# Kernel tuning notes

Hardware: AMD Instinct MI355X
Metric: run time of the kernel (lower is better)

The kernel has to match this reference:

```python
import jax, jax.numpy as jnp
import numpy as np

B = 65536
D_IN = 512
H = 512
EPS = 1e-5


def _layernorm(x, gamma, beta):
    # matches torch ref: unbiased std (ddof=1), eps added to std (not var)
    mean = jnp.mean(x, axis=-1, keepdims=True)
    std = jnp.std(x, axis=-1, ddof=1, keepdims=True)
    return gamma * (x - mean) / (std + EPS) + beta


def setup_inputs() -> dict:
    key = jax.random.key(0)
    ks = jax.random.split(key, 16)
    fan_in = D_IN + H
    s = 1.0 / np.sqrt(fan_in)
    inp = {
        "x": jax.random.normal(ks[0], (B, D_IN), dtype=jnp.float32),
        "prev_h": jax.random.normal(ks[1], (B, H), dtype=jnp.float32),
        "prev_c": jax.random.normal(ks[2], (B, H), dtype=jnp.float32),
        # torch Linear: weight [out, in], bias [out]
        "Wf": jax.random.uniform(ks[3], (H, fan_in), jnp.float32, -s, s),
        "bf": jax.random.uniform(ks[4], (H,), jnp.float32, -s, s),
        "Wi": jax.random.uniform(ks[5], (H, fan_in), jnp.float32, -s, s),
        "bi": jax.random.uniform(ks[6], (H,), jnp.float32, -s, s),
        "Wo": jax.random.uniform(ks[7], (H, fan_in), jnp.float32, -s, s),
        "bo": jax.random.uniform(ks[8], (H,), jnp.float32, -s, s),
        "Wj": jax.random.uniform(ks[9], (H, fan_in), jnp.float32, -s, s),
        "bj": jax.random.uniform(ks[10], (H,), jnp.float32, -s, s),
        "gamma_f": jnp.ones((H,), jnp.float32),
        "beta_f": jnp.zeros((H,), jnp.float32),
        "gamma_i": jnp.ones((H,), jnp.float32),
        "beta_i": jnp.zeros((H,), jnp.float32),
        "gamma_o": jnp.ones((H,), jnp.float32),
        "beta_o": jnp.zeros((H,), jnp.float32),
        "gamma_j": jnp.ones((H,), jnp.float32),
        "beta_j": jnp.zeros((H,), jnp.float32),
        "gamma_c": jnp.ones((H,), jnp.float32),
        "beta_c": jnp.zeros((H,), jnp.float32),
    }
    return inp


def reference(x, prev_h, prev_c, Wf, bf, Wi, bi, Wo, bo, Wj, bj,
              gamma_f, beta_f, gamma_i, beta_i, gamma_o, beta_o,
              gamma_j, beta_j, gamma_c, beta_c):
    combined = jnp.concatenate([x, prev_h], axis=-1)  # [B, D_IN+H]
    ft = jax.nn.sigmoid(_layernorm(combined @ Wf.T + bf, gamma_f, beta_f))
    it = jax.nn.sigmoid(_layernorm(combined @ Wi.T + bi, gamma_i, beta_i))
    ot = jax.nn.sigmoid(_layernorm(combined @ Wo.T + bo, gamma_o, beta_o))
    jt = jnp.tanh(_layernorm(combined @ Wj.T + bj, gamma_j, beta_j))
    c = ft * prev_c + jnp.minimum(1.0 - ft, it) * jt
    c = _layernorm(c, gamma_c, beta_c)
    h = ot * c
    return (h, c)
```

## Files before the change

### kernel.cpp

```cpp
#include <hip/hip_runtime.h>
#include <math.h>

#define B_ROWS 65536
#define D_IN   512
#define HDIM   512
#define FAN    1024
#define NCOL   2048
#define EPS    1e-5f

#define BM 256
#define BN 256
#define BK 64
#define KTILES (FAN / BK)
#define NITER  (KTILES / 2)
#define TILES_PER_BLK 4

typedef unsigned short u16;
using bfrag = __attribute__((ext_vector_type(8))) short;
using facc  = __attribute__((ext_vector_type(4))) float;
using us4   = __attribute__((ext_vector_type(4))) unsigned short;
using us8   = __attribute__((ext_vector_type(8))) unsigned short;

static __device__ __forceinline__ u16 f2b(float f) {
    unsigned u = __builtin_bit_cast(unsigned, f);
    u += 0x7fffu + ((u >> 16) & 1u);
    return (u16)(u >> 16);
}
static __device__ __forceinline__ float b2f(u16 h) {
    unsigned u = ((unsigned)h) << 16;
    return __builtin_bit_cast(float, u);
}
static __device__ __forceinline__ void gload16(const u16* g, u16* l) {
    __builtin_amdgcn_global_load_lds(
        (const __attribute__((address_space(1))) void*)g,
        (__attribute__((address_space(3))) void*)l, 16, 0, 0);
}
static __device__ __forceinline__ void wave_meanrstd(float s, float ss, float& mean, float& rstd)
{
#pragma unroll
    for (int o = 1; o < 64; o <<= 1) { s += __shfl_xor(s, o); ss += __shfl_xor(ss, o); }
    mean = s * (1.f / 512.f);
    float var = (ss - 512.f * mean * mean) * (1.f / 511.f);
    rstd = 1.f / (sqrtf(fmaxf(var, 0.f)) + EPS);
}
static __device__ __forceinline__ float fast_sigmoid(float z) {
    return __fdividef(1.f, 1.f + __expf(-z));
}
static __device__ __forceinline__ float fast_tanh(float z) {
    return __fdividef(2.f, 1.f + __expf(-2.f * z)) - 1.f;
}

__global__ void pack_combined(const float* __restrict__ x, const float* __restrict__ ph,
                              u16* __restrict__ comb)
{
    long i = (long)blockIdx.x * 256 + threadIdx.x;
    if (i >= (long)B_ROWS * D_IN / 4) return;
    long e = i * 4;
    long b = e >> 9;
    int  d = (int)(e & 511);
    float4 xv = *(const float4*)(x + e);
    float4 hv = *(const float4*)(ph + e);
    us4 xb = { f2b(xv.x), f2b(xv.y), f2b(xv.z), f2b(xv.w) };
    us4 hb = { f2b(hv.x), f2b(hv.y), f2b(hv.z), f2b(hv.w) };
    *(us4*)(comb + b * FAN + d)        = xb;
    *(us4*)(comb + b * FAN + D_IN + d) = hb;
}

__global__ void pack_w(const float* __restrict__ Wf, const float* __restrict__ Wi,
                       const float* __restrict__ Wo, const float* __restrict__ Wj,
                       u16* __restrict__ Wall)
{
    long i = (long)blockIdx.x * 256 + threadIdx.x;
    if (i >= (long)NCOL * FAN / 4) return;
    long e = i * 4;
    int  g = (int)(e >> 19);
    long rem = e & 524287L;
    const float* src = (g == 0) ? Wf : (g == 1) ? Wi : (g == 2) ? Wo : Wj;
    float4 v = *(const float4*)(src + rem);
    us4 p = { f2b(v.x), f2b(v.y), f2b(v.z), f2b(v.w) };
    *(us4*)(Wall + e) = p;
}

__global__ void pack_bias(const float* __restrict__ bf_, const float* __restrict__ bi_,
                          const float* __restrict__ bo_, const float* __restrict__ bj_,
                          float* __restrict__ biasAll)
{
    int idx = blockIdx.x * 256 + threadIdx.x;
    if (idx >= NCOL) return;
    int g = idx >> 9;
    const float* s = (g == 0) ? bf_ : (g == 1) ? bi_ : (g == 2) ? bo_ : bj_;
    biasAll[idx] = s[idx & 511];
}

__global__ __launch_bounds__(512)
void gemm_gates(const u16* __restrict__ A, const u16* __restrict__ W,
                const float* __restrict__ biasAll, u16* __restrict__ Cg)
{
    __shared__ u16 lds[2][4][8192];

    const int tid  = threadIdx.x;
    const int lane = tid & 63;
    const int wid  = tid >> 6;
    const int wm   = wid >> 2;
    const int wn   = wid & 3;

    const int nwg = gridDim.x;
    const int swz = (blockIdx.x & 7) * (nwg >> 3) + (blockIdx.x >> 3);
    const long bm  = swz >> 1;
    const int  bn4 = (swz & 1) * TILES_PER_BLK;
    const long arow0 = bm * BM;

    const int sr = tid >> 3;
    const int ss = tid & 7;

    facc acc[8][4];
#pragma unroll
    for (int i = 0; i < 8; ++i)
#pragma unroll
        for (int j = 0; j < 4; ++j) acc[i][j] = facc{0.f, 0.f, 0.f, 0.f};

    auto stageHalf = [&](int buf, int half, int ktg) {
        if (ktg >= TILES_PER_BLK * KTILES) ktg = 0;
        const long k0    = (long)(ktg & (KTILES - 1)) * BK;
        const long bcol0 = ((long)bn4 + (ktg >> 4)) * BN;
#pragma unroll
        for (int i = 0; i < 2; ++i) {
            const int r  = sr + i * 64;
            const int sx = ss ^ (r & 7);
            const u16* src = (half < 2)
                ? (A + (arow0 + half * 128 + r) * (long)FAN + k0 + sx * 8)
                : (W + (bcol0 + (half - 2) * 128 + r) * (long)FAN + k0 + sx * 8);
            gload16(src, &lds[buf][half][i * 4096 + wid * 512]);
        }
    };

    stageHalf(0, 0, 0); stageHalf(0, 1, 0); stageHalf(0, 2, 0); stageHalf(0, 3, 0);
    stageHalf(1, 2, 1); stageHalf(1, 3, 1);
    asm volatile("s_waitcnt vmcnt(4)" ::: "memory");
    __builtin_amdgcn_s_barrier();

    const u16* Ah[2] = { &lds[0][wm][0],            &lds[1][wm][0] };
    const u16* Bh[2] = { &lds[0][2 + (wn >> 1)][0], &lds[1][2 + (wn >> 1)][0] };
    const int lrB0 = (wn & 1) * 64;

#pragma unroll 1
    for (int tile = 0; tile < TILES_PER_BLK; ++tile) {
        const int kb = tile * KTILES;
#pragma unroll 1
        for (int t = 0; t < NITER; ++t) {
            bfrag bq[4][2];
#pragma unroll
            for (int p = 0; p < 8; ++p) {
                const int q  = p & 3;
                const int lt = p >> 2;
                bfrag aq[2][2];
                if (q == 0) {
#pragma unroll
                    for (int nf = 0; nf < 4; ++nf)
#pragma unroll
                        for (int kk = 0; kk < 2; ++kk) {
                            const int lr = lrB0 + nf * 16 + (lane & 15);
                            const int sl = (kk * 4 + (lane >> 4)) ^ (lane & 7);
                            bq[nf][kk] = *(const bfrag*)(Bh[lt] + lr * 64 + sl * 8);
                        }
                }
#pragma unroll
                for (int m2 = 0; m2 < 2; ++m2)
#pragma unroll
                    for (int kk = 0; kk < 2; ++kk) {
                        const int lr = (q * 2 + m2) * 16 + (lane & 15);
                        const int sl = (kk * 4 + (lane >> 4)) ^ (lane & 7);
                        aq[m2][kk] = *(const bfrag*)(Ah[lt] + lr * 64 + sl * 8);
                    }
                if (p == 0)      stageHalf(1, 0, kb + 2 * t + 1);
                else if (p == 1) stageHalf(1, 1, kb + 2 * t + 1);
                else if (p == 2) stageHalf(0, 2, kb + 2 * t + 2);
                else if (p == 3) stageHalf(0, 3, kb + 2 * t + 2);
                else if (p == 4) stageHalf(0, 0, kb + 2 * t + 2);
                else if (p == 5) stageHalf(0, 1, kb + 2 * t + 2);
                else if (p == 6) stageHalf(1, 2, kb + 2 * t + 3);
                else             stageHalf(1, 3, kb + 2 * t + 3);

                if (q == 0) asm volatile("s_waitcnt lgkmcnt(8)" ::: "memory");
                __builtin_amdgcn_s_barrier();
                asm volatile("s_waitcnt lgkmcnt(0)" ::: "memory");
                __builtin_amdgcn_s_setprio(1);
#pragma unroll
                for (int m2 = 0; m2 < 2; ++m2)
#pragma unroll
                    for (int nf = 0; nf < 4; ++nf)
#pragma unroll
                        for (int kk = 0; kk < 2; ++kk)
                            acc[q * 2 + m2][nf] = __builtin_amdgcn_mfma_f32_16x16x32_bf16(
                                bq[nf][kk], aq[m2][kk], acc[q * 2 + m2][nf], 0, 0, 0);
                __builtin_amdgcn_s_setprio(0);
                if (q == 3) asm volatile("s_waitcnt vmcnt(4)" ::: "memory");
                __builtin_amdgcn_s_barrier();
            }
        }

        const long bcol0 = ((long)bn4 + tile) * BN;
#pragma unroll
        for (int nf = 0; nf < 4; ++nf) {
            const long n = bcol0 + wn * 64 + nf * 16 + ((lane >> 4) << 2);
            float4 bv = *(const float4*)(biasAll + n);
#pragma unroll
            for (int mf = 0; mf < 8; ++mf) {
                const long m = arow0 + wm * 128 + mf * 16 + (lane & 15);
                us4 pk = { f2b(acc[mf][nf][0] + bv.x), f2b(acc[mf][nf][1] + bv.y),
                           f2b(acc[mf][nf][2] + bv.z), f2b(acc[mf][nf][3] + bv.w) };
                *(us4*)(Cg + m * (long)NCOL + n) = pk;
                acc[mf][nf] = facc{0.f, 0.f, 0.f, 0.f};
            }
        }
    }
}

__global__ __launch_bounds__(256)
void lstm_act(const u16* __restrict__ pre, const float* __restrict__ pc,
              const float* __restrict__ gf, const float* __restrict__ btf,
              const float* __restrict__ gi, const float* __restrict__ bti,
              const float* __restrict__ go, const float* __restrict__ bto,
              const float* __restrict__ gj, const float* __restrict__ btj,
              const float* __restrict__ gc, const float* __restrict__ btc,
              float* __restrict__ out_h, float* __restrict__ out_c, long rows)
{
    const int  lane = threadIdx.x & 63;
    const int  c0   = lane * 8;
    const long wave = (long)blockIdx.x * 4 + (threadIdx.x >> 6);
    const long totW = (long)gridDim.x * 4;

    const float* gs[4]  = { gf, gi, go, gj };
    const float* bts[4] = { btf, bti, bto, btj };
    float gg[4][8], tt[4][8], gcv[8], tcv[8];
#pragma unroll
    for (int g = 0; g < 4; ++g) {
        *(float4*)&gg[g][0] = *(const float4*)(gs[g] + c0);
        *(float4*)&gg[g][4] = *(const float4*)(gs[g] + c0 + 4);
        *(float4*)&tt[g][0] = *(const float4*)(bts[g] + c0);
        *(float4*)&tt[g][4] = *(const float4*)(bts[g] + c0 + 4);
    }
    *(float4*)&gcv[0] = *(const float4*)(gc + c0);
    *(float4*)&gcv[4] = *(const float4*)(gc + c0 + 4);
    *(float4*)&tcv[0] = *(const float4*)(btc + c0);
    *(float4*)&tcv[4] = *(const float4*)(btc + c0 + 4);

#pragma unroll 1
    for (long row = wave; row < rows; row += totW) {
        float a4[4][8];
#pragma unroll
        for (int g = 0; g < 4; ++g) {
            us8 pv = *(const us8*)(pre + row * NCOL + g * HDIM + c0);
            float y[8];
            float s = 0.f, ssum = 0.f;
#pragma unroll
            for (int e = 0; e < 8; ++e) {
                y[e] = b2f(pv[e]);
                s += y[e]; ssum += y[e] * y[e];
            }
            float mean, rstd;
            wave_meanrstd(s, ssum, mean, rstd);
#pragma unroll
            for (int e = 0; e < 8; ++e) {
                float z = (y[e] - mean) * rstd * gg[g][e] + tt[g][e];
                a4[g][e] = (g == 3) ? fast_tanh(z) : fast_sigmoid(z);
            }
        }

        float4 p0 = *(const float4*)(pc + row * HDIM + c0);
        float4 p1 = *(const float4*)(pc + row * HDIM + c0 + 4);
        float pcv[8] = { p0.x, p0.y, p0.z, p0.w, p1.x, p1.y, p1.z, p1.w };
        float cr[8];
        float s = 0.f, ssum = 0.f;
#pragma unroll
        for (int e = 0; e < 8; ++e) {
            cr[e] = a4[0][e] * pcv[e] + fminf(1.f - a4[0][e], a4[1][e]) * a4[3][e];
            s += cr[e]; ssum += cr[e] * cr[e];
        }
        float mean, rstd;
        wave_meanrstd(s, ssum, mean, rstd);
        float hv[8], cv[8];
#pragma unroll
        for (int e = 0; e < 8; ++e) {
            float cc = (cr[e] - mean) * rstd * gcv[e] + tcv[e];
            cv[e] = cc;
            hv[e] = a4[2][e] * cc;
        }
        *(float4*)(out_h + row * HDIM + c0)     = make_float4(hv[0], hv[1], hv[2], hv[3]);
        *(float4*)(out_h + row * HDIM + c0 + 4) = make_float4(hv[4], hv[5], hv[6], hv[7]);
        *(float4*)(out_c + row * HDIM + c0)     = make_float4(cv[0], cv[1], cv[2], cv[3]);
        *(float4*)(out_c + row * HDIM + c0 + 4) = make_float4(cv[4], cv[5], cv[6], cv[7]);
    }
}

static __device__ __forceinline__ void ln_pair(
    float y0, float y1,
    const float* __restrict__ gam, const float* __restrict__ bet, int c0,
    float* red, int lane, int wid, float& o0, float& o1)
{
    float s = y0 + y1, ss = y0 * y0 + y1 * y1;
#pragma unroll
    for (int o = 32; o; o >>= 1) { s += __shfl_down(s, o); ss += __shfl_down(ss, o); }
    if (lane == 0) { red[wid * 2] = s; red[wid * 2 + 1] = ss; }
    __syncthreads();
    float S  = red[0] + red[2] + red[4] + red[6];
    float SS = red[1] + red[3] + red[5] + red[7];
    __syncthreads();
    float mean = S * (1.f / 512.f);
    float var  = (SS - 512.f * mean * mean) * (1.f / 511.f);
    float rstd = 1.f / (sqrtf(fmaxf(var, 0.f)) + EPS);
    o0 = (y0 - mean) * rstd * gam[c0]     + bet[c0];
    o1 = (y1 - mean) * rstd * gam[c0 + 1] + bet[c0 + 1];
}

__global__ __launch_bounds__(256)
void lstm_naive(const float* __restrict__ x, const float* __restrict__ ph, const float* __restrict__ pc,
                const float* __restrict__ Wf, const float* __restrict__ bf_,
                const float* __restrict__ Wi, const float* __restrict__ bi_,
                const float* __restrict__ Wo, const float* __restrict__ bo_,
                const float* __restrict__ Wj, const float* __restrict__ bj_,
                const float* __restrict__ gf, const float* __restrict__ btf,
                const float* __restrict__ gi, const float* __restrict__ bti,
                const float* __restrict__ go, const float* __restrict__ bto,
                const float* __restrict__ gj, const float* __restrict__ btj,
                const float* __restrict__ gc, const float* __restrict__ btc,
                float* __restrict__ out_h, float* __restrict__ out_c)
{
    __shared__ float comb[FAN];
    __shared__ float red[8];
    const int b = blockIdx.x, t = threadIdx.x;
    const int lane = t & 63, wid = t >> 6;
    for (int k = t; k < D_IN; k += 256) {
        comb[k]        = x[(long)b * D_IN + k];
        comb[D_IN + k] = ph[(long)b * HDIM + k];
    }
    __syncthreads();
    const int c0 = t * 2;
    const float* Ws[4]  = { Wf, Wi, Wo, Wj };
    const float* bs[4]  = { bf_, bi_, bo_, bj_ };
    const float* gs[4]  = { gf, gi, go, gj };
    const float* bts[4] = { btf, bti, bto, btj };
    float a[4][2];
#pragma unroll
    for (int g = 0; g < 4; ++g) {
        float y[2];
#pragma unroll
        for (int e = 0; e < 2; ++e) {
            const float4* w4 = (const float4*)(Ws[g] + (long)(c0 + e) * FAN);
            const float4* c4 = (const float4*)comb;
            float s = 0.f;
            for (int k = 0; k < FAN / 4; ++k) {
                float4 wv = w4[k], cv = c4[k];
                s += wv.x * cv.x + wv.y * cv.y + wv.z * cv.z + wv.w * cv.w;
            }
            y[e] = s + bs[g][c0 + e];
        }
        ln_pair(y[0], y[1], gs[g], bts[g], c0, red, lane, wid, a[g][0], a[g][1]);
        if (g == 3) { a[g][0] = tanhf(a[g][0]); a[g][1] = tanhf(a[g][1]); }
        else        { a[g][0] = 1.f / (1.f + expf(-a[g][0]));
                      a[g][1] = 1.f / (1.f + expf(-a[g][1])); }
    }
    float2 pcv = *(const float2*)(pc + (long)b * HDIM + c0);
    float f0 = a[0][0], i0 = a[1][0], o0 = a[2][0], j0 = a[3][0];
    float f1 = a[0][1], i1 = a[1][1], o1 = a[2][1], j1 = a[3][1];
    float cr0 = f0 * pcv.x + fminf(1.f - f0, i0) * j0;
    float cr1 = f1 * pcv.y + fminf(1.f - f1, i1) * j1;
    float cc0, cc1;
    ln_pair(cr0, cr1, gc, btc, c0, red, lane, wid, cc0, cc1);
    *(float2*)(out_h + (long)b * HDIM + c0) = make_float2(o0 * cc0, o1 * cc1);
    *(float2*)(out_c + (long)b * HDIM + c0) = make_float2(cc0, cc1);
}

extern "C" void kernel_launch(void* const* d_in, const int* in_sizes, int n_in,
                              void* d_out, int out_size, void* d_ws, size_t ws_size,
                              hipStream_t stream)
{
    const float* x   = (const float*)d_in[0];
    const float* ph  = (const float*)d_in[1];
    const float* pc  = (const float*)d_in[2];
    const float* Wf  = (const float*)d_in[3];
    const float* bf_ = (const float*)d_in[4];
    const float* Wi  = (const float*)d_in[5];
    const float* bi_ = (const float*)d_in[6];
    const float* Wo  = (const float*)d_in[7];
    const float* bo_ = (const float*)d_in[8];
    const float* Wj  = (const float*)d_in[9];
    const float* bj_ = (const float*)d_in[10];
    const float* gf  = (const float*)d_in[11];
    const float* btf = (const float*)d_in[12];
    const float* gi  = (const float*)d_in[13];
    const float* bti = (const float*)d_in[14];
    const float* go  = (const float*)d_in[15];
    const float* bto = (const float*)d_in[16];
    const float* gj  = (const float*)d_in[17];
    const float* btj = (const float*)d_in[18];
    const float* gc  = (const float*)d_in[19];
    const float* btc = (const float*)d_in[20];
    float* out_h = (float*)d_out;
    float* out_c = out_h + (size_t)B_ROWS * HDIM;

    const size_t combElems  = (size_t)B_ROWS * FAN;
    const size_t wElems     = (size_t)NCOL * FAN;
    const size_t biasBytes  = (size_t)NCOL * sizeof(float);
    const size_t fixedBytes = (combElems + wElems) * 2 + biasBytes;

    long slabRows = 0;
    if (ws_size > fixedBytes) {
        size_t avail = ws_size - fixedBytes;
        slabRows = (long)(avail / ((size_t)NCOL * 2));
        slabRows &= ~1023L;
        if (slabRows > B_ROWS) slabRows = B_ROWS;
    }

    if (slabRows >= 1024) {
        u16*   comb    = (u16*)d_ws;
        u16*   Wall    = comb + combElems;
        float* biasAll = (float*)(Wall + wElems);
        u16*   pre     = (u16*)(biasAll + NCOL);
        pack_combined<<<dim3((unsigned)((B_ROWS * (long)D_IN / 4 + 255) / 256)), dim3(256), 0, stream>>>(x, ph, comb);
        pack_w<<<dim3((unsigned)(((long)NCOL * FAN / 4 + 255) / 256)), dim3(256), 0, stream>>>(Wf, Wi, Wo, Wj, Wall);
        pack_bias<<<dim3(8), dim3(256), 0, stream>>>(bf_, bi_, bo_, bj_, biasAll);
        for (long r0 = 0; r0 < B_ROWS; r0 += slabRows) {
            long rows = B_ROWS - r0; if (rows > slabRows) rows = slabRows;
            const unsigned nwg = (unsigned)((rows / BM) * 2);
            gemm_gates<<<dim3(nwg), dim3(512), 0, stream>>>(comb + r0 * FAN, Wall, biasAll, pre);
            lstm_act<<<dim3(1024), dim3(256), 0, stream>>>(
                pre, pc + r0 * HDIM,
                gf, btf, gi, bti, go, bto, gj, btj, gc, btc,
                out_h + r0 * HDIM, out_c + r0 * HDIM, rows);
        }
    } else {
        lstm_naive<<<dim3(B_ROWS), dim3(256), 0, stream>>>(
            x, ph, pc, Wf, bf_, Wi, bi_, Wo, bo_, Wj, bj_,
            gf, btf, gi, bti, go, bto, gj, btj, gc, btc, out_h, out_c);
    }
}
```

Baseline: 561.5 us.

## Switch gate GEMM to 32x32x16 MFMA, add nontemporal stores, double act grid

The gate GEMM inner loop now uses 32x32x16 bf16 MFMA instructions with 16-float accumulators instead of 16x16x32. Fragment loads and the LDS swizzle indexing are reworked to match, and the epilogue is rewritten for the new accumulator layout. The larger instruction does more work per issue and needs fewer LDS fragment reads. Separately, the activation kernel writes h and c with nontemporal stores and launches twice as many blocks. The new layout risks LDS bank conflicts and higher register pressure.

```diff
diff --git a/kernel.cpp b/kernel.cpp
--- a/kernel.cpp
+++ b/kernel.cpp
@@ -16,10 +16,11 @@
 #define TILES_PER_BLK 4
 
 typedef unsigned short u16;
-using bfrag = __attribute__((ext_vector_type(8))) short;
-using facc  = __attribute__((ext_vector_type(4))) float;
-using us4   = __attribute__((ext_vector_type(4))) unsigned short;
-using us8   = __attribute__((ext_vector_type(8))) unsigned short;
+using bfrag  = __attribute__((ext_vector_type(8))) short;
+using facc16 = __attribute__((ext_vector_type(16))) float;
+using us4    = __attribute__((ext_vector_type(4))) unsigned short;
+using us8    = __attribute__((ext_vector_type(8))) unsigned short;
+using f4v    = __attribute__((ext_vector_type(4))) float;
 
 static __device__ __forceinline__ u16 f2b(float f) {
     unsigned u = __builtin_bit_cast(unsigned, f);
@@ -113,11 +114,13 @@
     const int sr = tid >> 3;
     const int ss = tid & 7;
 
-    facc acc[8][4];
-#pragma unroll
-    for (int i = 0; i < 8; ++i)
-#pragma unroll
-        for (int j = 0; j < 4; ++j) acc[i][j] = facc{0.f, 0.f, 0.f, 0.f};
+    facc16 acc[4][2];
+#pragma unroll
+    for (int i = 0; i < 4; ++i)
+#pragma unroll
+        for (int j = 0; j < 2; ++j)
+#pragma unroll
+            for (int e = 0; e < 16; ++e) acc[i][j][e] = 0.f;
 
     auto stageHalf = [&](int buf, int half, int ktg) {
         if (ktg >= TILES_PER_BLK * KTILES) ktg = 0;
@@ -142,36 +145,36 @@
     const u16* Ah[2] = { &lds[0][wm][0],            &lds[1][wm][0] };
     const u16* Bh[2] = { &lds[0][2 + (wn >> 1)][0], &lds[1][2 + (wn >> 1)][0] };
     const int lrB0 = (wn & 1) * 64;
+    const int l31  = lane & 31;
+    const int h32  = lane >> 5;
 
 #pragma unroll 1
     for (int tile = 0; tile < TILES_PER_BLK; ++tile) {
         const int kb = tile * KTILES;
 #pragma unroll 1
         for (int t = 0; t < NITER; ++t) {
-            bfrag bq[4][2];
+            bfrag bq[2][4];
 #pragma unroll
             for (int p = 0; p < 8; ++p) {
                 const int q  = p & 3;
                 const int lt = p >> 2;
-                bfrag aq[2][2];
+                bfrag aq[4];
                 if (q == 0) {
 #pragma unroll
-                    for (int nf = 0; nf < 4; ++nf)
-#pragma unroll
-                        for (int kk = 0; kk < 2; ++kk) {
-                            const int lr = lrB0 + nf * 16 + (lane & 15);
-                            const int sl = (kk * 4 + (lane >> 4)) ^ (lane & 7);
-                            bq[nf][kk] = *(const bfrag*)(Bh[lt] + lr * 64 + sl * 8);
+                    for (int nf = 0; nf < 2; ++nf)
+#pragma unroll
+                        for (int ks = 0; ks < 4; ++ks) {
+                            const int lr = lrB0 + nf * 32 + l31;
+                            const int sl = (ks * 2 + h32) ^ (lr & 7);
+                            bq[nf][ks] = *(const bfrag*)(Bh[lt] + lr * 64 + sl * 8);
                         }
                 }
 #pragma unroll
-                for (int m2 = 0; m2 < 2; ++m2)
-#pragma unroll
-                    for (int kk = 0; kk < 2; ++kk) {
-                        const int lr = (q * 2 + m2) * 16 + (lane & 15);
-                        const int sl = (kk * 4 + (lane >> 4)) ^ (lane & 7);
-                        aq[m2][kk] = *(const bfrag*)(Ah[lt] + lr * 64 + sl * 8);
-                    }
+                for (int ks = 0; ks < 4; ++ks) {
+                    const int lr = q * 32 + l31;
+                    const int sl = (ks * 2 + h32) ^ (lr & 7);
+                    aq[ks] = *(const bfrag*)(Ah[lt] + lr * 64 + sl * 8);
+                }
                 if (p == 0)      stageHalf(1, 0, kb + 2 * t + 1);
                 else if (p == 1) stageHalf(1, 1, kb + 2 * t + 1);
                 else if (p == 2) stageHalf(0, 2, kb + 2 * t + 2);
@@ -186,13 +189,11 @@
                 asm volatile("s_waitcnt lgkmcnt(0)" ::: "memory");
                 __builtin_amdgcn_s_setprio(1);
 #pragma unroll
-                for (int m2 = 0; m2 < 2; ++m2)
-#pragma unroll
-                    for (int nf = 0; nf < 4; ++nf)
-#pragma unroll
-                        for (int kk = 0; kk < 2; ++kk)
-                            acc[q * 2 + m2][nf] = __builtin_amdgcn_mfma_f32_16x16x32_bf16(
-                                bq[nf][kk], aq[m2][kk], acc[q * 2 + m2][nf], 0, 0, 0);
+                for (int nf = 0; nf < 2; ++nf)
+#pragma unroll
+                    for (int ks = 0; ks < 4; ++ks)
+                        acc[q][nf] = __builtin_amdgcn_mfma_f32_32x32x16_bf16(
+                            bq[nf][ks], aq[ks], acc[q][nf], 0, 0, 0);
                 __builtin_amdgcn_s_setprio(0);
                 if (q == 3) asm volatile("s_waitcnt vmcnt(4)" ::: "memory");
                 __builtin_amdgcn_s_barrier();
@@ -200,19 +201,35 @@
         }
 
         const long bcol0 = ((long)bn4 + tile) * BN;
-#pragma unroll
-        for (int nf = 0; nf < 4; ++nf) {
-            const long n = bcol0 + wn * 64 + nf * 16 + ((lane >> 4) << 2);
-            float4 bv = *(const float4*)(biasAll + n);
-#pragma unroll
-            for (int mf = 0; mf < 8; ++mf) {
-                const long m = arow0 + wm * 128 + mf * 16 + (lane & 15);
-                us4 pk = { f2b(acc[mf][nf][0] + bv.x), f2b(acc[mf][nf][1] + bv.y),
-                           f2b(acc[mf][nf][2] + bv.z), f2b(acc[mf][nf][3] + bv.w) };
-                *(us4*)(Cg + m * (long)NCOL + n) = pk;
-                acc[mf][nf] = facc{0.f, 0.f, 0.f, 0.f};
-            }
-        }
+        float4 bias4[2][4];
+#pragma unroll
+        for (int nf = 0; nf < 2; ++nf)
+#pragma unroll
+            for (int g = 0; g < 4; ++g)
+                bias4[nf][g] = *(const float4*)(biasAll + bcol0 + wn * 64 + nf * 32
+                                                + g * 8 + (h32 << 2));
+#pragma unroll
+        for (int mf = 0; mf < 4; ++mf) {
+            const long m = arow0 + wm * 128 + mf * 32 + l31;
+            u16* rowp = Cg + m * (long)NCOL;
+#pragma unroll
+            for (int nf = 0; nf < 2; ++nf)
+#pragma unroll
+                for (int g = 0; g < 4; ++g) {
+                    const long n = bcol0 + wn * 64 + nf * 32 + g * 8 + (h32 << 2);
+                    us4 pk = { f2b(acc[mf][nf][4 * g + 0] + bias4[nf][g].x),
+                               f2b(acc[mf][nf][4 * g + 1] + bias4[nf][g].y),
+                               f2b(acc[mf][nf][4 * g + 2] + bias4[nf][g].z),
+                               f2b(acc[mf][nf][4 * g + 3] + bias4[nf][g].w) };
+                    *(us4*)(rowp + n) = pk;
+                }
+        }
+#pragma unroll
+        for (int i = 0; i < 4; ++i)
+#pragma unroll
+            for (int j = 0; j < 2; ++j)
+#pragma unroll
+                for (int e = 0; e < 16; ++e) acc[i][j][e] = 0.f;
     }
 }
 
@@ -286,10 +303,14 @@
             cv[e] = cc;
             hv[e] = a4[2][e] * cc;
         }
-        *(float4*)(out_h + row * HDIM + c0)     = make_float4(hv[0], hv[1], hv[2], hv[3]);
-        *(float4*)(out_h + row * HDIM + c0 + 4) = make_float4(hv[4], hv[5], hv[6], hv[7]);
-        *(float4*)(out_c + row * HDIM + c0)     = make_float4(cv[0], cv[1], cv[2], cv[3]);
-        *(float4*)(out_c + row * HDIM + c0 + 4) = make_float4(cv[4], cv[5], cv[6], cv[7]);
+        f4v h0 = { hv[0], hv[1], hv[2], hv[3] };
+        f4v h1 = { hv[4], hv[5], hv[6], hv[7] };
+        f4v c0v = { cv[0], cv[1], cv[2], cv[3] };
+        f4v c1v = { cv[4], cv[5], cv[6], cv[7] };
+        __builtin_nontemporal_store(h0,  (f4v*)(out_h + row * HDIM + c0));
+        __builtin_nontemporal_store(h1,  (f4v*)(out_h + row * HDIM + c0 + 4));
+        __builtin_nontemporal_store(c0v, (f4v*)(out_c + row * HDIM + c0));
+        __builtin_nontemporal_store(c1v, (f4v*)(out_c + row * HDIM + c0 + 4));
     }
 }
 
@@ -424,7 +445,7 @@
             long rows = B_ROWS - r0; if (rows > slabRows) rows = slabRows;
             const unsigned nwg = (unsigned)((rows / BM) * 2);
             gemm_gates<<<dim3(nwg), dim3(512), 0, stream>>>(comb + r0 * FAN, Wall, biasAll, pre);
-            lstm_act<<<dim3(1024), dim3(256), 0, stream>>>(
+            lstm_act<<<dim3(2048), dim3(256), 0, stream>>>(
                 pre, pc + r0 * HDIM,
                 gf, btf, gi, bti, go, bto, gj, btj, gc, btc,
                 out_h + r0 * HDIM, out_c + r0 * HDIM, rows);
```

Result: no change. 559.3 us (-0.4%).
